# Kernel optimization log

Hardware: AMD Instinct MI355X
Metric: run time of the kernel (lower is better)

Reference implementation:

```python
import jax, jax.numpy as jnp
import numpy as np

H = 16          # local heads
DN = 128        # qk_nope_head_dim
DR = 64         # qk_rope_head_dim
DV = 128        # v_head_dim
QL = 1536       # q_lora_rank
KVL = 512       # kv_lora_rank
HID = 5120      # hidden_size
T = 2048        # tokens
EPS = 1e-6
THETA = 10000.0
SCALE = (DN + DR) ** -0.5


def rmsnorm(x, w):
    return x * jax.lax.rsqrt(jnp.mean(x * x, axis=-1, keepdims=True) + EPS) * w


def rope_interleaved(x, pos):
    # non-neox (GPT-J interleaved) partial RoPE on last dim DR; x: [T, h, DR]
    inv_freq = 1.0 / (THETA ** (jnp.arange(0, DR, 2, dtype=jnp.float32) / DR))
    freqs = pos[:, None].astype(jnp.float32) * inv_freq          # [T, DR/2]
    cos = jnp.cos(freqs)[:, None, :]
    sin = jnp.sin(freqs)[:, None, :]
    x1, x2 = x[..., 0::2], x[..., 1::2]
    o1 = x1 * cos - x2 * sin
    o2 = x2 * cos + x1 * sin
    return jnp.stack([o1, o2], axis=-1).reshape(x.shape)


def setup_inputs() -> dict:
    key = jax.random.key(0)
    ks = jax.random.split(key, 8)
    s = lambda d: 1.0 / np.sqrt(d)
    return {
        "positions": jnp.arange(T, dtype=jnp.int64),
        "hidden_states": jax.random.normal(ks[0], (T, HID), jnp.float32),
        "wq_a": jax.random.normal(ks[1], (HID, QL), jnp.float32) * s(HID),
        "q_a_ln": jnp.ones((QL,), jnp.float32),
        "wq_b": jax.random.normal(ks[2], (QL, H * (DN + DR)), jnp.float32) * s(QL),
        "wkv_a": jax.random.normal(ks[3], (HID, KVL + DR), jnp.float32) * s(HID),
        "kv_a_ln": jnp.ones((KVL,), jnp.float32),
        "wkv_b": jax.random.normal(ks[4], (KVL, H * (DN + DV)), jnp.float32) * s(KVL),
        "wo": jax.random.normal(ks[5], (H * DV, HID), jnp.float32) * s(H * DV),
    }


def reference(positions, hidden_states, wq_a, q_a_ln, wq_b, wkv_a, kv_a_ln, wkv_b, wo):
    Tn = hidden_states.shape[0]
    # Q path: low-rank down, RMSNorm, up to per-head qk dims
    q = rmsnorm(hidden_states @ wq_a, q_a_ln) @ wq_b            # [T, H*(DN+DR)]
    q = q.reshape(Tn, H, DN + DR)
    q_nope, q_pe = q[..., :DN], q[..., DN:]
    # KV path: joint down-projection -> latent + shared rope key
    kv = hidden_states @ wkv_a                                   # [T, KVL+DR]
    c_kv, k_pe = kv[:, :KVL], kv[:, KVL:]
    c_kv = rmsnorm(c_kv, kv_a_ln)
    kvb = (c_kv @ wkv_b).reshape(Tn, H, DN + DV)
    k_nope, v = kvb[..., :DN], kvb[..., DN:]
    # partial RoPE on rope sub-dims only
    q_pe = rope_interleaved(q_pe, positions)                     # [T, H, DR]
    k_pe = rope_interleaved(k_pe[:, None, :], positions)         # [T, 1, DR]
    # causal attention over full qk_head_dim
    scores = (jnp.einsum('thd,shd->hts', q_nope, k_nope)
              + jnp.einsum('thd,sod->hts', q_pe, k_pe)) * SCALE  # [H, T, T]
    mask = jnp.tril(jnp.ones((Tn, Tn), bool))
    scores = jnp.where(mask[None], scores, jnp.finfo(scores.dtype).min)
    attn = jax.nn.softmax(scores, axis=-1)
    out = jnp.einsum('hts,shd->thd', attn, v).reshape(Tn, H * DV)
    return out @ wo                                              # [T, HID]
```

## Files before the change

kernel.cpp:

```cpp
#include <hip/hip_runtime.h>
#include <hip/hip_bf16.h>

typedef __attribute__((ext_vector_type(8))) short bf16x8;
typedef __attribute__((ext_vector_type(4))) float f32x4;

typedef __attribute__((address_space(1))) const unsigned int gu32;
typedef __attribute__((address_space(3))) unsigned int lu32;

#define ATTN_SCALE 0.07216878364870323f

static __device__ __forceinline__ float bf2f(__hip_bfloat16 b) { return __bfloat162float(b); }

__global__ void cvt_kernel(const float* __restrict__ in, __hip_bfloat16* __restrict__ out, int n) {
  for (int i = (blockIdx.x * 256 + threadIdx.x) * 4; i < n; i += gridDim.x * 256 * 4) {
    float4 v = *(const float4*)(in + i);
    out[i + 0] = __float2bfloat16(v.x);
    out[i + 1] = __float2bfloat16(v.y);
    out[i + 2] = __float2bfloat16(v.z);
    out[i + 3] = __float2bfloat16(v.w);
  }
}

__global__ void transpose_cvt_kernel(const float* __restrict__ in, __hip_bfloat16* __restrict__ out,
                                     int R, int C) {
  __shared__ float tile[32][33];
  int bi = blockIdx.x, bj = blockIdx.y;
  int tx = threadIdx.x & 31, ty = threadIdx.x >> 5;
#pragma unroll
  for (int k2 = 0; k2 < 4; k2++) {
    int r = bi * 32 + ty + k2 * 8;
    tile[ty + k2 * 8][tx] = in[(size_t)r * C + bj * 32 + tx];
  }
  __syncthreads();
#pragma unroll
  for (int k2 = 0; k2 < 4; k2++) {
    int cc = bj * 32 + ty + k2 * 8;
    out[(size_t)cc * R + bi * 32 + tx] = __float2bfloat16(tile[tx][ty + k2 * 8]);
  }
}

__global__ void rmsnorm_kernel(const float* __restrict__ in, int in_stride, int cols,
                               const float* __restrict__ wgt,
                               __hip_bfloat16* __restrict__ out, int out_stride) {
  int row = blockIdx.x;
  const float* x = in + (size_t)row * in_stride;
  float ss = 0.f;
  for (int c = threadIdx.x; c < cols; c += 256) { float v = x[c]; ss += v * v; }
#pragma unroll
  for (int d = 1; d < 64; d <<= 1) ss += __shfl_xor(ss, d, 64);
  __shared__ float red[4];
  if ((threadIdx.x & 63) == 0) red[threadIdx.x >> 6] = ss;
  __syncthreads();
  float tot = red[0] + red[1] + red[2] + red[3];
  float r = rsqrtf(tot / cols + 1e-6f);
  __hip_bfloat16* o = out + (size_t)row * out_stride;
  for (int c = threadIdx.x; c < cols; c += 256)
    o[c] = __float2bfloat16(x[c] * r * wgt[c]);
}

__global__ void rope_q_kernel(__hip_bfloat16* __restrict__ q) {
  int row = blockIdx.x;
#pragma unroll
  for (int jj = 0; jj < 2; jj++) {
    int v = threadIdx.x + 256 * jj;
    int h = v >> 5, i = v & 31;
    float inv = powf(10000.f, -(2.f * i) / 64.f);
    float fr = (float)row * inv;
    float s, c;
    sincosf(fr, &s, &c);
    __hip_bfloat16* p = q + (size_t)row * 3072 + h * 192 + 128 + 2 * i;
    float x1 = bf2f(p[0]), x2 = bf2f(p[1]);
    p[0] = __float2bfloat16(x1 * c - x2 * s);
    p[1] = __float2bfloat16(x2 * c + x1 * s);
  }
}

__global__ void rope_k_kernel(const float* __restrict__ src, int stride,
                              __hip_bfloat16* __restrict__ kpe) {
  int row = blockIdx.x;
  int i = threadIdx.x;
  if (i < 32) {
    float inv = powf(10000.f, -(2.f * i) / 64.f);
    float fr = (float)row * inv;
    float s, c;
    sincosf(fr, &s, &c);
    float x1 = src[(size_t)row * stride + 2 * i];
    float x2 = src[(size_t)row * stride + 2 * i + 1];
    kpe[(size_t)row * 64 + 2 * i]     = __float2bfloat16(x1 * c - x2 * s);
    kpe[(size_t)row * 64 + 2 * i + 1] = __float2bfloat16(x2 * c + x1 * s);
  }
}

template <bool OUT_BF16>
__global__ __launch_bounds__(256, 2) void gemm_lds_kernel(
    const __hip_bfloat16* __restrict__ A, const __hip_bfloat16* __restrict__ Bt,
    void* __restrict__ Cout, int M, int N, int K) {
  __shared__ __hip_bfloat16 As[2][128][32];
  __shared__ __hip_bfloat16 Bs[2][128][32];
  const int t = threadIdx.x;
  const int w = t >> 6, l = t & 63;
  const int lr = l & 15, lh = l >> 4;
  const int wr = w >> 1, wc = w & 1;
  const int bm = blockIdx.x, bn = blockIdx.y;

  const int r0 = l >> 2;
  const int c0 = (l & 3) * 8;
  const int rowA0 = w * 16 + r0;
  const int rowA1 = (4 + w) * 16 + r0;
  const __hip_bfloat16* Ag0 = A + (size_t)(bm * 128 + rowA0) * K + c0;
  const __hip_bfloat16* Ag1 = A + (size_t)(bm * 128 + rowA1) * K + c0;
  int br0 = bn * 128 + rowA0; if (br0 >= N) br0 = N - 1;
  int br1 = bn * 128 + rowA1; if (br1 >= N) br1 = N - 1;
  const __hip_bfloat16* Bg0 = Bt + (size_t)br0 * K + c0;
  const __hip_bfloat16* Bg1 = Bt + (size_t)br1 * K + c0;

  f32x4 acc[4][4];
#pragma unroll
  for (int i = 0; i < 4; i++)
#pragma unroll
    for (int j = 0; j < 4; j++) acc[i][j] = f32x4{0.f, 0.f, 0.f, 0.f};

  auto issue = [&](int kt, int buf) {
    const int ko = kt * 32;
    __builtin_amdgcn_global_load_lds((gu32*)(Ag0 + ko), (lu32*)&As[buf][rowA0][c0], 16, 0, 0);
    __builtin_amdgcn_global_load_lds((gu32*)(Ag1 + ko), (lu32*)&As[buf][rowA1][c0], 16, 0, 0);
    __builtin_amdgcn_global_load_lds((gu32*)(Bg0 + ko), (lu32*)&Bs[buf][rowA0][c0], 16, 0, 0);
    __builtin_amdgcn_global_load_lds((gu32*)(Bg1 + ko), (lu32*)&Bs[buf][rowA1][c0], 16, 0, 0);
  };

  const int KT = K >> 5;
  issue(0, 0);
  int cur = 0;
  for (int kt = 0; kt < KT; ++kt) {
    __syncthreads();
    if (kt + 1 < KT) issue(kt + 1, cur ^ 1);
    bf16x8 af[4], bff[4];
#pragma unroll
    for (int m = 0; m < 4; m++) af[m] = *(bf16x8*)&As[cur][wr * 64 + m * 16 + lr][lh * 8];
#pragma unroll
    for (int n = 0; n < 4; n++) bff[n] = *(bf16x8*)&Bs[cur][wc * 64 + n * 16 + lr][lh * 8];
    __builtin_amdgcn_s_setprio(1);
#pragma unroll
    for (int m = 0; m < 4; m++)
#pragma unroll
      for (int n = 0; n < 4; n++)
        acc[m][n] = __builtin_amdgcn_mfma_f32_16x16x32_bf16(af[m], bff[n], acc[m][n], 0, 0, 0);
    __builtin_amdgcn_s_setprio(0);
    cur ^= 1;
  }
#pragma unroll
  for (int m = 0; m < 4; m++) {
    int row = bm * 128 + wr * 64 + m * 16 + lh * 4;
#pragma unroll
    for (int n = 0; n < 4; n++) {
      int col = bn * 128 + wc * 64 + n * 16 + lr;
      if (col < N) {
#pragma unroll
        for (int j = 0; j < 4; j++) {
          if (OUT_BF16)
            ((__hip_bfloat16*)Cout)[(size_t)(row + j) * N + col] = __float2bfloat16(acc[m][n][j]);
          else
            ((float*)Cout)[(size_t)(row + j) * N + col] = acc[m][n][j];
        }
      }
    }
  }
}

__global__ __launch_bounds__(256, 2) void attn_kernel(
    const __hip_bfloat16* __restrict__ Q, const __hip_bfloat16* __restrict__ KVB,
    const __hip_bfloat16* __restrict__ KPE, __hip_bfloat16* __restrict__ Out) {
  __shared__ __hip_bfloat16 Ks[64][200];
  __shared__ __hip_bfloat16 Vs[128][72];
  __shared__ __hip_bfloat16 Ps[4][16][72];

  const int t = threadIdx.x;
  const int w = t >> 6, l = t & 63;
  const int lr = l & 15, lh = l >> 4;
  const int bm = (int)gridDim.x - 1 - (int)blockIdx.x;
  const int h = blockIdx.y;

  bf16x8 aq[6];
  const int qrow = bm * 64 + w * 16 + lr;
  const __hip_bfloat16* qp = Q + (size_t)qrow * 3072 + h * 192 + lh * 8;
#pragma unroll
  for (int ks = 0; ks < 6; ks++) aq[ks] = *(const bf16x8*)(qp + ks * 32);

  f32x4 o_acc[8];
#pragma unroll
  for (int i = 0; i < 8; i++) o_acc[i] = f32x4{0.f, 0.f, 0.f, 0.f};
  float m_run[4], l_run[4];
#pragma unroll
  for (int j = 0; j < 4; j++) { m_run[j] = -INFINITY; l_run[j] = 0.f; }

  for (int kb = 0; kb <= bm; ++kb) {
    const int s0 = kb * 64;
#pragma unroll
    for (int j = 0; j < 6; j++) {
      int c = t + 256 * j;
      int row = c / 24;
      int col8 = (c % 24) * 8;
      const __hip_bfloat16* src;
      if (col8 < 128) src = KVB + (size_t)(s0 + row) * 4096 + h * 256 + col8;
      else            src = KPE + (size_t)(s0 + row) * 64 + (col8 - 128);
      *(bf16x8*)&Ks[row][col8] = *(const bf16x8*)src;
    }
#pragma unroll
    for (int j = 0; j < 4; j++) {
      int c = t + 256 * j;
      int srow = c >> 4;
      int dv8 = (c & 15) * 8;
      bf16x8 v = *(const bf16x8*)(KVB + (size_t)(s0 + srow) * 4096 + h * 256 + 128 + dv8);
      int sc = srow >> 3, sl = srow & 7;
#pragma unroll
      for (int i = 0; i < 8; i++) {
        int dv = dv8 + i;
        Vs[dv][((sc ^ ((dv >> 3) & 7)) << 3) | sl] = ((__hip_bfloat16*)&v)[i];
      }
    }
    __syncthreads();

    f32x4 sa[4];
#pragma unroll
    for (int nf = 0; nf < 4; nf++) sa[nf] = f32x4{0.f, 0.f, 0.f, 0.f};
#pragma unroll
    for (int ks = 0; ks < 6; ks++) {
#pragma unroll
      for (int nf = 0; nf < 4; nf++) {
        bf16x8 b = *(bf16x8*)&Ks[nf * 16 + lr][ks * 32 + lh * 8];
        sa[nf] = __builtin_amdgcn_mfma_f32_16x16x32_bf16(aq[ks], b, sa[nf], 0, 0, 0);
      }
    }
    float sv[4][4];
    const bool diag = (kb == bm);
#pragma unroll
    for (int nf = 0; nf < 4; nf++) {
      int scol = s0 + nf * 16 + lr;
#pragma unroll
      for (int j = 0; j < 4; j++) {
        float x = sa[nf][j] * ATTN_SCALE;
        if (diag) {
          int qr = bm * 64 + w * 16 + lh * 4 + j;
          if (scol > qr) x = -1e30f;
        }
        sv[nf][j] = x;
      }
    }
    float pm[4], fac[4];
#pragma unroll
    for (int j = 0; j < 4; j++) {
      float mx = fmaxf(fmaxf(sv[0][j], sv[1][j]), fmaxf(sv[2][j], sv[3][j]));
#pragma unroll
      for (int d = 1; d < 16; d <<= 1) mx = fmaxf(mx, __shfl_xor(mx, d, 64));
      float mn = fmaxf(m_run[j], mx);
      fac[j] = __expf(m_run[j] - mn);
      m_run[j] = mn;
      pm[j] = mn;
    }
    float rs[4] = {0.f, 0.f, 0.f, 0.f};
#pragma unroll
    for (int nf = 0; nf < 4; nf++) {
#pragma unroll
      for (int j = 0; j < 4; j++) {
        float p = __expf(sv[nf][j] - pm[j]);
        rs[j] += p;
        Ps[w][lh * 4 + j][nf * 16 + lr] = __float2bfloat16(p);
      }
    }
#pragma unroll
    for (int j = 0; j < 4; j++) {
      float s = rs[j];
#pragma unroll
      for (int d = 1; d < 16; d <<= 1) s += __shfl_xor(s, d, 64);
      l_run[j] = l_run[j] * fac[j] + s;
    }
#pragma unroll
    for (int nf = 0; nf < 8; nf++)
#pragma unroll
      for (int j = 0; j < 4; j++) o_acc[nf][j] *= fac[j];

#pragma unroll
    for (int ks = 0; ks < 2; ks++) {
      bf16x8 pa = *(bf16x8*)&Ps[w][lr][ks * 32 + lh * 8];
#pragma unroll
      for (int nf = 0; nf < 8; nf++) {
        int dv = nf * 16 + lr;
        int c8 = ks * 4 + lh;
        bf16x8 vb = *(bf16x8*)&Vs[dv][((c8 ^ ((dv >> 3) & 7)) << 3)];
        o_acc[nf] = __builtin_amdgcn_mfma_f32_16x16x32_bf16(pa, vb, o_acc[nf], 0, 0, 0);
      }
    }
    __syncthreads();
  }
#pragma unroll
  for (int nf = 0; nf < 8; nf++) {
    int col = h * 128 + nf * 16 + lr;
#pragma unroll
    for (int j = 0; j < 4; j++) {
      int row = bm * 64 + w * 16 + lh * 4 + j;
      Out[(size_t)row * 2048 + col] = __float2bfloat16(o_acc[nf][j] / l_run[j]);
    }
  }
}

extern "C" void kernel_launch(void* const* d_in, const int* in_sizes, int n_in,
                              void* d_out, int out_size, void* d_ws, size_t ws_size,
                              hipStream_t stream) {
  const float* hidden  = (const float*)d_in[1];
  const float* wq_a    = (const float*)d_in[2];
  const float* q_a_ln  = (const float*)d_in[3];
  const float* wq_b    = (const float*)d_in[4];
  const float* wkv_a   = (const float*)d_in[5];
  const float* kv_a_ln = (const float*)d_in[6];
  const float* wkv_b   = (const float*)d_in[7];
  const float* wo      = (const float*)d_in[8];
  float* out = (float*)d_out;

  char* ws = (char*)d_ws;
  size_t off = 0;
  auto alloc = [&](size_t bytes) { void* p = ws + off; off += (bytes + 255) & ~(size_t)255; return p; };
  __hip_bfloat16* h_bf    = (__hip_bfloat16*)alloc((size_t)2048 * 5120 * 2);
  __hip_bfloat16* qkvw_t  = (__hip_bfloat16*)alloc((size_t)2112 * 5120 * 2);
  __hip_bfloat16* wq_b_t  = (__hip_bfloat16*)alloc((size_t)3072 * 1536 * 2);
  __hip_bfloat16* wkv_b_t = (__hip_bfloat16*)alloc((size_t)4096 * 512 * 2);
  __hip_bfloat16* wo_t    = (__hip_bfloat16*)alloc((size_t)5120 * 2048 * 2);
  float*          qkv_lat = (float*)alloc((size_t)2048 * 2112 * 4);
  __hip_bfloat16* q_a_bf  = (__hip_bfloat16*)alloc((size_t)2048 * 1536 * 2);
  __hip_bfloat16* ckv_bf  = (__hip_bfloat16*)alloc((size_t)2048 * 512 * 2);
  __hip_bfloat16* kpe_bf  = (__hip_bfloat16*)alloc((size_t)2048 * 64 * 2);
  __hip_bfloat16* q_bf    = (__hip_bfloat16*)alloc((size_t)2048 * 3072 * 2);
  __hip_bfloat16* kvb_bf  = (__hip_bfloat16*)alloc((size_t)2048 * 4096 * 2);
  __hip_bfloat16* attn_o  = (__hip_bfloat16*)alloc((size_t)2048 * 2048 * 2);
  (void)ws_size; (void)in_sizes; (void)n_in; (void)out_size;

  cvt_kernel<<<1024, 256, 0, stream>>>(hidden, h_bf, 2048 * 5120);
  transpose_cvt_kernel<<<dim3(160, 48), 256, 0, stream>>>(wq_a, qkvw_t, 5120, 1536);
  transpose_cvt_kernel<<<dim3(160, 18), 256, 0, stream>>>(wkv_a, qkvw_t + (size_t)1536 * 5120, 5120, 576);
  transpose_cvt_kernel<<<dim3(48, 96), 256, 0, stream>>>(wq_b, wq_b_t, 1536, 3072);
  transpose_cvt_kernel<<<dim3(16, 128), 256, 0, stream>>>(wkv_b, wkv_b_t, 512, 4096);
  transpose_cvt_kernel<<<dim3(64, 160), 256, 0, stream>>>(wo, wo_t, 2048, 5120);

  gemm_lds_kernel<false><<<dim3(16, 17), 256, 0, stream>>>(h_bf, qkvw_t, qkv_lat, 2048, 2112, 5120);

  rmsnorm_kernel<<<2048, 256, 0, stream>>>(qkv_lat, 2112, 1536, q_a_ln, q_a_bf, 1536);
  rmsnorm_kernel<<<2048, 256, 0, stream>>>(qkv_lat + 1536, 2112, 512, kv_a_ln, ckv_bf, 512);
  rope_k_kernel<<<2048, 64, 0, stream>>>(qkv_lat + 2048, 2112, kpe_bf);

  gemm_lds_kernel<true><<<dim3(16, 24), 256, 0, stream>>>(q_a_bf, wq_b_t, q_bf, 2048, 3072, 1536);
  rope_q_kernel<<<2048, 256, 0, stream>>>(q_bf);

  gemm_lds_kernel<true><<<dim3(16, 32), 256, 0, stream>>>(ckv_bf, wkv_b_t, kvb_bf, 2048, 4096, 512);

  attn_kernel<<<dim3(32, 16), 256, 0, stream>>>(q_bf, kvb_bf, kpe_bf, attn_o);

  gemm_lds_kernel<false><<<dim3(16, 40), 256, 0, stream>>>(attn_o, wo_t, out, 2048, 5120, 2048);
}
```

Baseline: 547.9 us.

## Emit split K-nope and transposed V from kv_b GEMM; prefetch attention tiles in registers

The kv_b GEMM epilogue now writes K-nope into its own contiguous buffer and V pre-transposed (head-dim major) with packed 4-wide stores. This lets the attention kernel load V with vectorized 16-byte copies instead of scattering eight scalar LDS writes per element. Attention also prefetches the next K/V tile into registers while computing on the current one. The costs are strided transposed stores in the GEMM epilogue and extra register pressure in attention.

Result: no change. 545.3 us (-0.5%).

```diff
diff --git a/kernel.cpp b/kernel.cpp
--- a/kernel.cpp
+++ b/kernel.cpp
@@ -2,6 +2,7 @@
 #include <hip/hip_bf16.h>
 
 typedef __attribute__((ext_vector_type(8))) short bf16x8;
+typedef __attribute__((ext_vector_type(4))) short bf16x4;
 typedef __attribute__((ext_vector_type(4))) float f32x4;
 
 typedef __attribute__((address_space(1))) const unsigned int gu32;
@@ -91,10 +92,11 @@
   }
 }
 
-template <bool OUT_BF16>
+template <int MODE>
 __global__ __launch_bounds__(256, 2) void gemm_lds_kernel(
     const __hip_bfloat16* __restrict__ A, const __hip_bfloat16* __restrict__ Bt,
-    void* __restrict__ Cout, int M, int N, int K) {
+    void* __restrict__ Cout, __hip_bfloat16* __restrict__ KnopeOut,
+    __hip_bfloat16* __restrict__ VtOut, int M, int N, int K) {
   __shared__ __hip_bfloat16 As[2][128][32];
   __shared__ __hip_bfloat16 Bs[2][128][32];
   const int t = threadIdx.x;
@@ -154,10 +156,26 @@
 #pragma unroll
     for (int n = 0; n < 4; n++) {
       int col = bn * 128 + wc * 64 + n * 16 + lr;
-      if (col < N) {
+      if (MODE == 2) {
+        int hcol = ((col >> 8) << 7) + (col & 127);
+        if ((bn & 1) == 0) {
+#pragma unroll
+          for (int j = 0; j < 4; j++)
+            KnopeOut[(size_t)(row + j) * 2048 + hcol] = __float2bfloat16(acc[m][n][j]);
+        } else {
+          bf16x4 pk;
+#pragma unroll
+          for (int j = 0; j < 4; j++) {
+            union { __hip_bfloat16 b; short s; } cv;
+            cv.b = __float2bfloat16(acc[m][n][j]);
+            pk[j] = cv.s;
+          }
+          *(bf16x4*)(VtOut + (size_t)hcol * 2048 + row) = pk;
+        }
+      } else if (col < N) {
 #pragma unroll
         for (int j = 0; j < 4; j++) {
-          if (OUT_BF16)
+          if (MODE == 1)
             ((__hip_bfloat16*)Cout)[(size_t)(row + j) * N + col] = __float2bfloat16(acc[m][n][j]);
           else
             ((float*)Cout)[(size_t)(row + j) * N + col] = acc[m][n][j];
@@ -168,8 +186,9 @@
 }
 
 __global__ __launch_bounds__(256, 2) void attn_kernel(
-    const __hip_bfloat16* __restrict__ Q, const __hip_bfloat16* __restrict__ KVB,
-    const __hip_bfloat16* __restrict__ KPE, __hip_bfloat16* __restrict__ Out) {
+    const __hip_bfloat16* __restrict__ Q, const __hip_bfloat16* __restrict__ Knope,
+    const __hip_bfloat16* __restrict__ Vt, const __hip_bfloat16* __restrict__ KPE,
+    __hip_bfloat16* __restrict__ Out) {
   __shared__ __hip_bfloat16 Ks[64][200];
   __shared__ __hip_bfloat16 Vs[128][72];
   __shared__ __hip_bfloat16 Ps[4][16][72];
@@ -181,10 +200,12 @@
   const int h = blockIdx.y;
 
   bf16x8 aq[6];
-  const int qrow = bm * 64 + w * 16 + lr;
-  const __hip_bfloat16* qp = Q + (size_t)qrow * 3072 + h * 192 + lh * 8;
-#pragma unroll
-  for (int ks = 0; ks < 6; ks++) aq[ks] = *(const bf16x8*)(qp + ks * 32);
+  {
+    const int qrow = bm * 64 + w * 16 + lr;
+    const __hip_bfloat16* qp = Q + (size_t)qrow * 3072 + h * 192 + lh * 8;
+#pragma unroll
+    for (int ks = 0; ks < 6; ks++) aq[ks] = *(const bf16x8*)(qp + ks * 32);
+  }
 
   f32x4 o_acc[8];
 #pragma unroll
@@ -193,32 +214,47 @@
 #pragma unroll
   for (int j = 0; j < 4; j++) { m_run[j] = -INFINITY; l_run[j] = 0.f; }
 
+  bf16x8 kreg[6], vreg[4];
+  auto load_regs = [&](int kb) {
+    const int s0 = kb * 64;
+#pragma unroll
+    for (int j = 0; j < 6; j++) {
+      int c = t + 256 * j;
+      int row = c / 24, col8 = (c % 24) * 8;
+      const __hip_bfloat16* src = (col8 < 128)
+          ? Knope + (size_t)(s0 + row) * 2048 + h * 128 + col8
+          : KPE + (size_t)(s0 + row) * 64 + (col8 - 128);
+      kreg[j] = *(const bf16x8*)src;
+    }
+#pragma unroll
+    for (int j = 0; j < 4; j++) {
+      int c = t + 256 * j;
+      int dv = c >> 3;
+      int sc = c & 7;
+      vreg[j] = *(const bf16x8*)(Vt + (size_t)(h * 128 + dv) * 2048 + s0 + sc * 8);
+    }
+  };
+  auto store_tile = [&]() {
+#pragma unroll
+    for (int j = 0; j < 6; j++) {
+      int c = t + 256 * j;
+      int row = c / 24, col8 = (c % 24) * 8;
+      *(bf16x8*)&Ks[row][col8] = kreg[j];
+    }
+#pragma unroll
+    for (int j = 0; j < 4; j++) {
+      int c = t + 256 * j;
+      int dv = c >> 3, sc = c & 7;
+      *(bf16x8*)&Vs[dv][(sc ^ ((dv >> 3) & 7)) << 3] = vreg[j];
+    }
+  };
+
+  load_regs(0);
   for (int kb = 0; kb <= bm; ++kb) {
     const int s0 = kb * 64;
-#pragma unroll
-    for (int j = 0; j < 6; j++) {
-      int c = t + 256 * j;
-      int row = c / 24;
-      int col8 = (c % 24) * 8;
-      const __hip_bfloat16* src;
-      if (col8 < 128) src = KVB + (size_t)(s0 + row) * 4096 + h * 256 + col8;
-      else            src = KPE + (size_t)(s0 + row) * 64 + (col8 - 128);
-      *(bf16x8*)&Ks[row][col8] = *(const bf16x8*)src;
-    }
-#pragma unroll
-    for (int j = 0; j < 4; j++) {
-      int c = t + 256 * j;
-      int srow = c >> 4;
-      int dv8 = (c & 15) * 8;
-      bf16x8 v = *(const bf16x8*)(KVB + (size_t)(s0 + srow) * 4096 + h * 256 + 128 + dv8);
-      int sc = srow >> 3, sl = srow & 7;
-#pragma unroll
-      for (int i = 0; i < 8; i++) {
-        int dv = dv8 + i;
-        Vs[dv][((sc ^ ((dv >> 3) & 7)) << 3) | sl] = ((__hip_bfloat16*)&v)[i];
-      }
-    }
+    store_tile();
     __syncthreads();
+    if (kb < bm) load_regs(kb + 1);
 
     f32x4 sa[4];
 #pragma unroll
@@ -319,18 +355,19 @@
   char* ws = (char*)d_ws;
   size_t off = 0;
   auto alloc = [&](size_t bytes) { void* p = ws + off; off += (bytes + 255) & ~(size_t)255; return p; };
-  __hip_bfloat16* h_bf    = (__hip_bfloat16*)alloc((size_t)2048 * 5120 * 2);
-  __hip_bfloat16* qkvw_t  = (__hip_bfloat16*)alloc((size_t)2112 * 5120 * 2);
-  __hip_bfloat16* wq_b_t  = (__hip_bfloat16*)alloc((size_t)3072 * 1536 * 2);
-  __hip_bfloat16* wkv_b_t = (__hip_bfloat16*)alloc((size_t)4096 * 512 * 2);
-  __hip_bfloat16* wo_t    = (__hip_bfloat16*)alloc((size_t)5120 * 2048 * 2);
-  float*          qkv_lat = (float*)alloc((size_t)2048 * 2112 * 4);
-  __hip_bfloat16* q_a_bf  = (__hip_bfloat16*)alloc((size_t)2048 * 1536 * 2);
-  __hip_bfloat16* ckv_bf  = (__hip_bfloat16*)alloc((size_t)2048 * 512 * 2);
-  __hip_bfloat16* kpe_bf  = (__hip_bfloat16*)alloc((size_t)2048 * 64 * 2);
-  __hip_bfloat16* q_bf    = (__hip_bfloat16*)alloc((size_t)2048 * 3072 * 2);
-  __hip_bfloat16* kvb_bf  = (__hip_bfloat16*)alloc((size_t)2048 * 4096 * 2);
-  __hip_bfloat16* attn_o  = (__hip_bfloat16*)alloc((size_t)2048 * 2048 * 2);
+  __hip_bfloat16* h_bf     = (__hip_bfloat16*)alloc((size_t)2048 * 5120 * 2);
+  __hip_bfloat16* qkvw_t   = (__hip_bfloat16*)alloc((size_t)2112 * 5120 * 2);
+  __hip_bfloat16* wq_b_t   = (__hip_bfloat16*)alloc((size_t)3072 * 1536 * 2);
+  __hip_bfloat16* wkv_b_t  = (__hip_bfloat16*)alloc((size_t)4096 * 512 * 2);
+  __hip_bfloat16* wo_t     = (__hip_bfloat16*)alloc((size_t)5120 * 2048 * 2);
+  float*          qkv_lat  = (float*)alloc((size_t)2048 * 2112 * 4);
+  __hip_bfloat16* q_a_bf   = (__hip_bfloat16*)alloc((size_t)2048 * 1536 * 2);
+  __hip_bfloat16* ckv_bf   = (__hip_bfloat16*)alloc((size_t)2048 * 512 * 2);
+  __hip_bfloat16* kpe_bf   = (__hip_bfloat16*)alloc((size_t)2048 * 64 * 2);
+  __hip_bfloat16* q_bf     = (__hip_bfloat16*)alloc((size_t)2048 * 3072 * 2);
+  __hip_bfloat16* knope_bf = (__hip_bfloat16*)alloc((size_t)2048 * 2048 * 2);
+  __hip_bfloat16* vt_bf    = (__hip_bfloat16*)alloc((size_t)2048 * 2048 * 2);
+  __hip_bfloat16* attn_o   = (__hip_bfloat16*)alloc((size_t)2048 * 2048 * 2);
   (void)ws_size; (void)in_sizes; (void)n_in; (void)out_size;
 
   cvt_kernel<<<1024, 256, 0, stream>>>(hidden, h_bf, 2048 * 5120);
@@ -340,18 +377,22 @@
   transpose_cvt_kernel<<<dim3(16, 128), 256, 0, stream>>>(wkv_b, wkv_b_t, 512, 4096);
   transpose_cvt_kernel<<<dim3(64, 160), 256, 0, stream>>>(wo, wo_t, 2048, 5120);
 
-  gemm_lds_kernel<false><<<dim3(16, 17), 256, 0, stream>>>(h_bf, qkvw_t, qkv_lat, 2048, 2112, 5120);
+  gemm_lds_kernel<0><<<dim3(16, 17), 256, 0, stream>>>(h_bf, qkvw_t, qkv_lat, nullptr, nullptr,
+                                                       2048, 2112, 5120);
 
   rmsnorm_kernel<<<2048, 256, 0, stream>>>(qkv_lat, 2112, 1536, q_a_ln, q_a_bf, 1536);
   rmsnorm_kernel<<<2048, 256, 0, stream>>>(qkv_lat + 1536, 2112, 512, kv_a_ln, ckv_bf, 512);
   rope_k_kernel<<<2048, 64, 0, stream>>>(qkv_lat + 2048, 2112, kpe_bf);
 
-  gemm_lds_kernel<true><<<dim3(16, 24), 256, 0, stream>>>(q_a_bf, wq_b_t, q_bf, 2048, 3072, 1536);
+  gemm_lds_kernel<1><<<dim3(16, 24), 256, 0, stream>>>(q_a_bf, wq_b_t, q_bf, nullptr, nullptr,
+                                                       2048, 3072, 1536);
   rope_q_kernel<<<2048, 256, 0, stream>>>(q_bf);
 
-  gemm_lds_kernel<true><<<dim3(16, 32), 256, 0, stream>>>(ckv_bf, wkv_b_t, kvb_bf, 2048, 4096, 512);
-
-  attn_kernel<<<dim3(32, 16), 256, 0, stream>>>(q_bf, kvb_bf, kpe_bf, attn_o);
-
-  gemm_lds_kernel<false><<<dim3(16, 40), 256, 0, stream>>>(attn_o, wo_t, out, 2048, 5120, 2048);
-}
+  gemm_lds_kernel<2><<<dim3(16, 32), 256, 0, stream>>>(ckv_bf, wkv_b_t, nullptr, knope_bf, vt_bf,
+                                                       2048, 4096, 512);
+
+  attn_kernel<<<dim3(32, 16), 256, 0, stream>>>(q_bf, knope_bf, vt_bf, kpe_bf, attn_o);
+
+  gemm_lds_kernel<0><<<dim3(16, 40), 256, 0, stream>>>(attn_o, wo_t, out, nullptr, nullptr,
+                                                       2048, 5120, 2048);
+}
```
